# Kernel tuning notes

Hardware: AMD Instinct MI355X
Metric: run time of the kernel (lower is better)

The kernel has to match this reference:

```python
import jax, jax.numpy as jnp
import numpy as np

B, CIN, COUT, H, W, K = 4, 3, 16, 256, 256, 5
PAD = K // 2  # replicate padding keeps spatial size


def _dilation_sum(x, w):
    """Learnable dilation, channel_merge_mode='sum'.
    x: (B,Cin,H,W), w: (Cout,Cin,K,K).
    out[b,o,i,j] = sum_c max_{di,dj} ( x_pad[b,c,i+di,j+dj] + w[o,c,di,dj] )
    """
    xp = jnp.pad(x, ((0, 0), (0, 0), (PAD, PAD), (PAD, PAD)), mode='edge')
    acc = jnp.full((x.shape[0], w.shape[0], x.shape[1], H, W), -jnp.inf, dtype=x.dtype)
    for di in range(K):  # fixed small kernel loop (unrolled), not a data-dim loop
        for dj in range(K):
            win = xp[:, :, di:di + H, dj:dj + W]                     # (B,Cin,H,W)
            cand = win[:, None] + w[None, :, :, di, dj][:, :, :, None, None]  # (B,Cout,Cin,H,W)
            acc = jnp.maximum(acc, cand)
    return acc.sum(axis=2)  # merge over input channels -> (B,Cout,H,W)


def _erosion_identity(y, w):
    """Learnable erosion, channel_merge_mode='identity' (each channel independent).
    y: (B,Cout,H,W), w: (Cout,K,K).
    out[b,o,i,j] = min_{di,dj} ( y_pad[b,o,i+di,j+dj] - w[o,di,dj] )
    """
    yp = jnp.pad(y, ((0, 0), (0, 0), (PAD, PAD), (PAD, PAD)), mode='edge')
    acc = jnp.full(y.shape, jnp.inf, dtype=y.dtype)
    for di in range(K):
        for dj in range(K):
            acc = jnp.minimum(acc, yp[:, :, di:di + H, dj:dj + W] - w[None, :, di, dj, None, None])
    return acc


def setup_inputs() -> dict:
    key = jax.random.key(0)
    k1, k2, k3 = jax.random.split(key, 3)
    x = jax.random.normal(k1, (B, CIN, H, W), dtype=jnp.float32)
    w_d = jax.random.normal(k2, (COUT, CIN, K, K), dtype=jnp.float32) * 0.05
    w_e = jax.random.normal(k3, (COUT, K, K), dtype=jnp.float32) * 0.05
    return {"x": x, "w_d": w_d, "w_e": w_e}


def reference(x, w_d, w_e):
    # Closing = dilation (max-plus, sum merge) followed by erosion (min-plus, identity merge)
    dilated = _dilation_sum(x, w_d)
    return _erosion_identity(dilated, w_e)
```

## Files before the change

kernel.cpp:

```cpp
#include <hip/hip_runtime.h>


typedef _Float16 h2 __attribute__((ext_vector_type(2)));

namespace {
constexpr int HH = 256, WW = 256, CI = 3;
constexpr int XS2 = 36;
constexpr int CH2 = 68 * XS2;
constexpr int DS2 = 36;
}

struct __align__(16) H4  { h2 a, b, c, d; };
struct __align__(8)  H2p { h2 a, b; };

__device__ __forceinline__ h2 pmax(h2 a, h2 b) { return __builtin_elementwise_max(a, b); }
__device__ __forceinline__ h2 pmin(h2 a, h2 b) { return __builtin_elementwise_min(a, b); }

__device__ __forceinline__ h2 shr1(h2 lo, h2 hi) {
    unsigned a = __builtin_bit_cast(unsigned, lo);
    unsigned b = __builtin_bit_cast(unsigned, hi);
    return __builtin_bit_cast(h2, (a >> 16) | (b << 16));
}

__device__ __forceinline__ h2 splat2(float f) {
    auto p = __builtin_amdgcn_cvt_pkrtz(f, f);
    return __builtin_bit_cast(h2, p);
}

__device__ __forceinline__ void erode_one(int t, const h2* sd, const float* ew,
                                          float* outz, int i0, int j0) {
    const int r = t / 5, s = t - r * 5;
    const int eb = r * DS2 + 6 * s;
    h2 n0 = splat2(60000.f), n1 = n0, n2 = n0, n3 = n0, n4 = n0, n5 = n0;
#pragma unroll
    for (int r5 = 0; r5 < 5; ++r5) {
        const H2p q0 = *(const H2p*)&sd[eb + r5 * DS2];
        const H2p q1 = *(const H2p*)&sd[eb + r5 * DS2 + 2];
        const H2p q2 = *(const H2p*)&sd[eb + r5 * DS2 + 4];
        const H2p q3 = *(const H2p*)&sd[eb + r5 * DS2 + 6];
        const h2 e0 = q0.a, e1 = q0.b, e2 = q1.a, e3 = q1.b,
                 e4 = q2.a, e5 = q2.b, e6 = q3.a, e7 = q3.b;
        const h2 t0 = shr1(e0, e1), t1 = shr1(e1, e2), t2 = shr1(e2, e3),
                 t3 = shr1(e3, e4), t4 = shr1(e4, e5), t5 = shr1(e5, e6),
                 t6 = shr1(e6, e7);
        const h2 w0 = splat2(-ew[r5*5+0]), w1 = splat2(-ew[r5*5+1]),
                 w2 = splat2(-ew[r5*5+2]), w3 = splat2(-ew[r5*5+3]),
                 w4 = splat2(-ew[r5*5+4]);
        n0 = pmin(n0, pmin(pmin(e0 + w0, t0 + w1), pmin(e1 + w2, pmin(t1 + w3, e2 + w4))));
        n1 = pmin(n1, pmin(pmin(e1 + w0, t1 + w1), pmin(e2 + w2, pmin(t2 + w3, e3 + w4))));
        n2 = pmin(n2, pmin(pmin(e2 + w0, t2 + w1), pmin(e3 + w2, pmin(t3 + w3, e4 + w4))));
        n3 = pmin(n3, pmin(pmin(e3 + w0, t3 + w1), pmin(e4 + w2, pmin(t4 + w3, e5 + w4))));
        n4 = pmin(n4, pmin(pmin(e4 + w0, t4 + w1), pmin(e5 + w2, pmin(t5 + w3, e6 + w4))));
        n5 = pmin(n5, pmin(pmin(e5 + w0, t5 + w1), pmin(e6 + w2, pmin(t6 + w3, e7 + w4))));
    }
    float* op = outz + ((size_t)(i0 + r) << 8) + j0 + 12 * s;
    *(float4*)op       = make_float4((float)n0.x, (float)n0.y, (float)n1.x, (float)n1.y);
    *(float4*)(op + 4) = make_float4((float)n2.x, (float)n2.y, (float)n3.x, (float)n3.y);
    *(float4*)(op + 8) = make_float4((float)n4.x, (float)n4.y, (float)n5.x, (float)n5.y);
}

__global__ __launch_bounds__(256, 4)
void closing_v10(const float* __restrict__ x, const float* __restrict__ wd,
                 const float* __restrict__ we, float* __restrict__ out) {
    __shared__ __align__(16) h2 sx2[CI * CH2];
    __shared__ __align__(16) h2 sd2[64 * DS2];

    const int tid = threadIdx.x;
    const int bx = blockIdx.x, by = blockIdx.y, z = blockIdx.z;
    const int o = z & 15, b = z >> 4;
    const int i0 = min(by * 60, HH - 60);
    const int j0 = min(bx * 60, WW - 60);
    const float* xb = x + (size_t)b * (CI * HH * WW);

#pragma unroll
    for (int k = 0; k < 14; ++k) {
        const int idx = tid + (k << 8);
        if (idx < 3468) {
            const int c   = idx / 1156;
            const int rem = idx - c * 1156;
            const int r   = rem / 17;
            const int q   = rem - r * 17;
            const int gi  = min(max(i0 - 4 + r, 0), HH - 1);
            const int gj0 = j0 - 4 + (q << 2);
            const float* rowp = xb + c * (HH * WW) + (gi << 8);
            float4 v;
            if (gj0 < 0)        { const float t = rowp[0];      v = make_float4(t, t, t, t); }
            else if (gj0 > 252) { const float t = rowp[WW - 1]; v = make_float4(t, t, t, t); }
            else                  v = *(const float4*)(rowp + gj0);
            H2p hw;
            hw.a = h2{(_Float16)v.x, (_Float16)v.y};
            hw.b = h2{(_Float16)v.z, (_Float16)v.w};
            *(H2p*)&sx2[c * CH2 + r * XS2 + (q << 1)] = hw;
        }
    }
    __syncthreads();

    {
        const int r = tid >> 2, s = tid & 3;
        h2 acc0 = splat2(0.f), acc1 = acc0, acc2 = acc0, acc3 = acc0,
           acc4 = acc0, acc5 = acc0, acc6 = acc0, acc7 = acc0;
#pragma unroll
        for (int c = 0; c < CI; ++c) {
            const float* wr = wd + (o * CI + c) * 25;
            h2 m0 = splat2(-60000.f), m1 = m0, m2 = m0, m3 = m0,
               m4 = m0, m5 = m0, m6 = m0, m7 = m0;
            const int base = c * CH2 + r * XS2 + (s << 3);
#pragma unroll
            for (int r5 = 0; r5 < 5; ++r5) {
                const H4  A = *(const H4*)&sx2[base + r5 * XS2];
                const H4  B = *(const H4*)&sx2[base + r5 * XS2 + 4];
                const H2p C = *(const H2p*)&sx2[base + r5 * XS2 + 8];
                const h2 h0 = A.a, h1 = A.b, h2_ = A.c, h3 = A.d,
                         h4 = B.a, h5 = B.b, h6 = B.c, h7 = B.d,
                         h8 = C.a, h9 = C.b;
                const h2 t0 = shr1(h0, h1), t1 = shr1(h1, h2_), t2 = shr1(h2_, h3),
                         t3 = shr1(h3, h4), t4 = shr1(h4, h5), t5 = shr1(h5, h6),
                         t6 = shr1(h6, h7), t7 = shr1(h7, h8), t8 = shr1(h8, h9);
                const h2 w0 = splat2(wr[r5*5+0]), w1 = splat2(wr[r5*5+1]),
                         w2 = splat2(wr[r5*5+2]), w3 = splat2(wr[r5*5+3]),
                         w4 = splat2(wr[r5*5+4]);
                m0 = pmax(m0, pmax(pmax(h0 + w0, t0 + w1), pmax(h1 + w2, pmax(t1 + w3, h2_ + w4))));
                m1 = pmax(m1, pmax(pmax(h1 + w0, t1 + w1), pmax(h2_ + w2, pmax(t2 + w3, h3 + w4))));
                m2 = pmax(m2, pmax(pmax(h2_ + w0, t2 + w1), pmax(h3 + w2, pmax(t3 + w3, h4 + w4))));
                m3 = pmax(m3, pmax(pmax(h3 + w0, t3 + w1), pmax(h4 + w2, pmax(t4 + w3, h5 + w4))));
                m4 = pmax(m4, pmax(pmax(h4 + w0, t4 + w1), pmax(h5 + w2, pmax(t5 + w3, h6 + w4))));
                m5 = pmax(m5, pmax(pmax(h5 + w0, t5 + w1), pmax(h6 + w2, pmax(t6 + w3, h7 + w4))));
                m6 = pmax(m6, pmax(pmax(h6 + w0, t6 + w1), pmax(h7 + w2, pmax(t7 + w3, h8 + w4))));
                m7 = pmax(m7, pmax(pmax(h7 + w0, t7 + w1), pmax(h8 + w2, pmax(t8 + w3, h9 + w4))));
            }
            acc0 = acc0 + m0; acc1 = acc1 + m1; acc2 = acc2 + m2; acc3 = acc3 + m3;
            acc4 = acc4 + m4; acc5 = acc5 + m5; acc6 = acc6 + m6; acc7 = acc7 + m7;
        }
        if (j0 == 0       && s == 0) acc0 = (h2)acc1.x;
        if (j0 == WW - 60 && s == 3) acc7 = (h2)acc6.y;
        const bool top = (i0 == 0), bot = (i0 == HH - 60);
        if (!((top && r < 2) || (bot && r > 61))) {
            const H4 p0 = {acc0, acc1, acc2, acc3};
            const H4 p1 = {acc4, acc5, acc6, acc7};
            const int db = r * DS2 + (s << 3);
            *(H4*)&sd2[db]     = p0;
            *(H4*)&sd2[db + 4] = p1;
            if (top && r == 2) {
                *(H4*)&sd2[0 * DS2 + (s << 3)]     = p0;
                *(H4*)&sd2[0 * DS2 + (s << 3) + 4] = p1;
                *(H4*)&sd2[1 * DS2 + (s << 3)]     = p0;
                *(H4*)&sd2[1 * DS2 + (s << 3) + 4] = p1;
            }
            if (bot && r == 61) {
                *(H4*)&sd2[62 * DS2 + (s << 3)]     = p0;
                *(H4*)&sd2[62 * DS2 + (s << 3) + 4] = p1;
                *(H4*)&sd2[63 * DS2 + (s << 3)]     = p0;
                *(H4*)&sd2[63 * DS2 + (s << 3) + 4] = p1;
            }
        }
    }
    __syncthreads();

    {
        const float* ew = we + o * 25;
        float* outz = out + ((size_t)z << 16);
        erode_one(tid, sd2, ew, outz, i0, j0);
        if (tid < 44) erode_one(tid + 256, sd2, ew, outz, i0, j0);
    }
}

extern "C" void kernel_launch(void* const* d_in, const int* in_sizes, int n_in,
                              void* d_out, int out_size, void* d_ws, size_t ws_size,
                              hipStream_t stream) {
    const float* x  = (const float*)d_in[0];
    const float* wd = (const float*)d_in[1];
    const float* we = (const float*)d_in[2];
    float* out = (float*)d_out;

    dim3 grid(5, 5, 64);
    closing_v10<<<grid, dim3(256), 0, stream>>>(x, wd, we, out);
}
```

Measured before the change: 96.95 us.

## Shrink output tiles to 32x48 and rebalance per-thread work across stages

Output tiles shrink from 60x60 to 32 rows by 48 columns, so the grid grows from 5x5x64 to 6x8x64 blocks. The shared-memory buffers are resized to match. Each dilation thread now computes 4 packed pairs instead of 8, and each erosion thread computes 3 pairs instead of 6, so every thread does one erosion task rather than some doing a second. The aim is more blocks and a more even workload, with less per-thread register pressure and less tail imbalance. In exchange, more halo rows and columns are recomputed and reloaded relative to useful output, and the output stores become narrower float2 writes.

```diff
diff --git a/kernel.cpp b/kernel.cpp
--- a/kernel.cpp
+++ b/kernel.cpp
@@ -5,9 +5,9 @@
 
 namespace {
 constexpr int HH = 256, WW = 256, CI = 3;
-constexpr int XS2 = 36;
-constexpr int CH2 = 68 * XS2;
-constexpr int DS2 = 36;
+constexpr int XS2 = 28;
+constexpr int CH2 = 40 * XS2;
+constexpr int DS2 = 28;
 }
 
 struct __align__(16) H4  { h2 a, b, c, d; };
@@ -27,59 +27,27 @@
     return __builtin_bit_cast(h2, p);
 }
 
-__device__ __forceinline__ void erode_one(int t, const h2* sd, const float* ew,
-                                          float* outz, int i0, int j0) {
-    const int r = t / 5, s = t - r * 5;
-    const int eb = r * DS2 + 6 * s;
-    h2 n0 = splat2(60000.f), n1 = n0, n2 = n0, n3 = n0, n4 = n0, n5 = n0;
-#pragma unroll
-    for (int r5 = 0; r5 < 5; ++r5) {
-        const H2p q0 = *(const H2p*)&sd[eb + r5 * DS2];
-        const H2p q1 = *(const H2p*)&sd[eb + r5 * DS2 + 2];
-        const H2p q2 = *(const H2p*)&sd[eb + r5 * DS2 + 4];
-        const H2p q3 = *(const H2p*)&sd[eb + r5 * DS2 + 6];
-        const h2 e0 = q0.a, e1 = q0.b, e2 = q1.a, e3 = q1.b,
-                 e4 = q2.a, e5 = q2.b, e6 = q3.a, e7 = q3.b;
-        const h2 t0 = shr1(e0, e1), t1 = shr1(e1, e2), t2 = shr1(e2, e3),
-                 t3 = shr1(e3, e4), t4 = shr1(e4, e5), t5 = shr1(e5, e6),
-                 t6 = shr1(e6, e7);
-        const h2 w0 = splat2(-ew[r5*5+0]), w1 = splat2(-ew[r5*5+1]),
-                 w2 = splat2(-ew[r5*5+2]), w3 = splat2(-ew[r5*5+3]),
-                 w4 = splat2(-ew[r5*5+4]);
-        n0 = pmin(n0, pmin(pmin(e0 + w0, t0 + w1), pmin(e1 + w2, pmin(t1 + w3, e2 + w4))));
-        n1 = pmin(n1, pmin(pmin(e1 + w0, t1 + w1), pmin(e2 + w2, pmin(t2 + w3, e3 + w4))));
-        n2 = pmin(n2, pmin(pmin(e2 + w0, t2 + w1), pmin(e3 + w2, pmin(t3 + w3, e4 + w4))));
-        n3 = pmin(n3, pmin(pmin(e3 + w0, t3 + w1), pmin(e4 + w2, pmin(t4 + w3, e5 + w4))));
-        n4 = pmin(n4, pmin(pmin(e4 + w0, t4 + w1), pmin(e5 + w2, pmin(t5 + w3, e6 + w4))));
-        n5 = pmin(n5, pmin(pmin(e5 + w0, t5 + w1), pmin(e6 + w2, pmin(t6 + w3, e7 + w4))));
-    }
-    float* op = outz + ((size_t)(i0 + r) << 8) + j0 + 12 * s;
-    *(float4*)op       = make_float4((float)n0.x, (float)n0.y, (float)n1.x, (float)n1.y);
-    *(float4*)(op + 4) = make_float4((float)n2.x, (float)n2.y, (float)n3.x, (float)n3.y);
-    *(float4*)(op + 8) = make_float4((float)n4.x, (float)n4.y, (float)n5.x, (float)n5.y);
-}
-
 __global__ __launch_bounds__(256, 4)
-void closing_v10(const float* __restrict__ x, const float* __restrict__ wd,
+void closing_v13(const float* __restrict__ x, const float* __restrict__ wd,
                  const float* __restrict__ we, float* __restrict__ out) {
-    __shared__ __align__(16) h2 sx2[CI * CH2];
-    __shared__ __align__(16) h2 sd2[64 * DS2];
+    __shared__ __align__(16) h2 sx2[CI * CH2 + 8];
+    __shared__ __align__(16) h2 sd2[36 * DS2];
 
     const int tid = threadIdx.x;
     const int bx = blockIdx.x, by = blockIdx.y, z = blockIdx.z;
     const int o = z & 15, b = z >> 4;
-    const int i0 = min(by * 60, HH - 60);
-    const int j0 = min(bx * 60, WW - 60);
+    const int i0 = by * 32;
+    const int j0 = min(bx * 48, WW - 48);
     const float* xb = x + (size_t)b * (CI * HH * WW);
 
 #pragma unroll
-    for (int k = 0; k < 14; ++k) {
+    for (int k = 0; k < 7; ++k) {
         const int idx = tid + (k << 8);
-        if (idx < 3468) {
-            const int c   = idx / 1156;
-            const int rem = idx - c * 1156;
-            const int r   = rem / 17;
-            const int q   = rem - r * 17;
+        if (idx < 1680) {
+            const int c   = idx / 560;
+            const int rem = idx - c * 560;
+            const int r   = rem / 14;
+            const int q   = rem - r * 14;
             const int gi  = min(max(i0 - 4 + r, 0), HH - 1);
             const int gj0 = j0 - 4 + (q << 2);
             const float* rowp = xb + c * (HH * WW) + (gi << 8);
@@ -95,27 +63,21 @@
     }
     __syncthreads();
 
-    {
-        const int r = tid >> 2, s = tid & 3;
-        h2 acc0 = splat2(0.f), acc1 = acc0, acc2 = acc0, acc3 = acc0,
-           acc4 = acc0, acc5 = acc0, acc6 = acc0, acc7 = acc0;
+    if (tid < 252) {
+        const int r = tid / 7, s = tid - r * 7;
+        h2 acc0 = splat2(0.f), acc1 = acc0, acc2 = acc0, acc3 = acc0;
 #pragma unroll
         for (int c = 0; c < CI; ++c) {
             const float* wr = wd + (o * CI + c) * 25;
-            h2 m0 = splat2(-60000.f), m1 = m0, m2 = m0, m3 = m0,
-               m4 = m0, m5 = m0, m6 = m0, m7 = m0;
-            const int base = c * CH2 + r * XS2 + (s << 3);
+            h2 m0 = splat2(-60000.f), m1 = m0, m2 = m0, m3 = m0;
+            const int base = c * CH2 + r * XS2 + (s << 2);
 #pragma unroll
             for (int r5 = 0; r5 < 5; ++r5) {
                 const H4  A = *(const H4*)&sx2[base + r5 * XS2];
-                const H4  B = *(const H4*)&sx2[base + r5 * XS2 + 4];
-                const H2p C = *(const H2p*)&sx2[base + r5 * XS2 + 8];
-                const h2 h0 = A.a, h1 = A.b, h2_ = A.c, h3 = A.d,
-                         h4 = B.a, h5 = B.b, h6 = B.c, h7 = B.d,
-                         h8 = C.a, h9 = C.b;
+                const H2p B = *(const H2p*)&sx2[base + r5 * XS2 + 4];
+                const h2 h0 = A.a, h1 = A.b, h2_ = A.c, h3 = A.d, h4 = B.a, h5 = B.b;
                 const h2 t0 = shr1(h0, h1), t1 = shr1(h1, h2_), t2 = shr1(h2_, h3),
-                         t3 = shr1(h3, h4), t4 = shr1(h4, h5), t5 = shr1(h5, h6),
-                         t6 = shr1(h6, h7), t7 = shr1(h7, h8), t8 = shr1(h8, h9);
+                         t3 = shr1(h3, h4), t4 = shr1(h4, h5);
                 const h2 w0 = splat2(wr[r5*5+0]), w1 = splat2(wr[r5*5+1]),
                          w2 = splat2(wr[r5*5+2]), w3 = splat2(wr[r5*5+3]),
                          w4 = splat2(wr[r5*5+4]);
@@ -123,44 +85,61 @@
                 m1 = pmax(m1, pmax(pmax(h1 + w0, t1 + w1), pmax(h2_ + w2, pmax(t2 + w3, h3 + w4))));
                 m2 = pmax(m2, pmax(pmax(h2_ + w0, t2 + w1), pmax(h3 + w2, pmax(t3 + w3, h4 + w4))));
                 m3 = pmax(m3, pmax(pmax(h3 + w0, t3 + w1), pmax(h4 + w2, pmax(t4 + w3, h5 + w4))));
-                m4 = pmax(m4, pmax(pmax(h4 + w0, t4 + w1), pmax(h5 + w2, pmax(t5 + w3, h6 + w4))));
-                m5 = pmax(m5, pmax(pmax(h5 + w0, t5 + w1), pmax(h6 + w2, pmax(t6 + w3, h7 + w4))));
-                m6 = pmax(m6, pmax(pmax(h6 + w0, t6 + w1), pmax(h7 + w2, pmax(t7 + w3, h8 + w4))));
-                m7 = pmax(m7, pmax(pmax(h7 + w0, t7 + w1), pmax(h8 + w2, pmax(t8 + w3, h9 + w4))));
             }
             acc0 = acc0 + m0; acc1 = acc1 + m1; acc2 = acc2 + m2; acc3 = acc3 + m3;
-            acc4 = acc4 + m4; acc5 = acc5 + m5; acc6 = acc6 + m6; acc7 = acc7 + m7;
         }
         if (j0 == 0       && s == 0) acc0 = (h2)acc1.x;
-        if (j0 == WW - 60 && s == 3) acc7 = (h2)acc6.y;
-        const bool top = (i0 == 0), bot = (i0 == HH - 60);
-        if (!((top && r < 2) || (bot && r > 61))) {
-            const H4 p0 = {acc0, acc1, acc2, acc3};
-            const H4 p1 = {acc4, acc5, acc6, acc7};
-            const int db = r * DS2 + (s << 3);
-            *(H4*)&sd2[db]     = p0;
-            *(H4*)&sd2[db + 4] = p1;
+        if (j0 == WW - 48 && s == 6) acc1 = (h2)acc0.y;
+        const bool top = (by == 0), bot = (by == 7);
+        if (!((top && r < 2) || (bot && r > 33))) {
+            const int db = r * DS2 + (s << 2);
+            if (s < 6) { const H4 p = {acc0, acc1, acc2, acc3}; *(H4*)&sd2[db] = p; }
+            else       { const H2p p = {acc0, acc1};            *(H2p*)&sd2[db] = p; }
             if (top && r == 2) {
-                *(H4*)&sd2[0 * DS2 + (s << 3)]     = p0;
-                *(H4*)&sd2[0 * DS2 + (s << 3) + 4] = p1;
-                *(H4*)&sd2[1 * DS2 + (s << 3)]     = p0;
-                *(H4*)&sd2[1 * DS2 + (s << 3) + 4] = p1;
+                if (s < 6) { const H4 p = {acc0, acc1, acc2, acc3};
+                             *(H4*)&sd2[0 * DS2 + (s << 2)] = p;
+                             *(H4*)&sd2[1 * DS2 + (s << 2)] = p; }
+                else       { const H2p p = {acc0, acc1};
+                             *(H2p*)&sd2[0 * DS2 + (s << 2)] = p;
+                             *(H2p*)&sd2[1 * DS2 + (s << 2)] = p; }
             }
-            if (bot && r == 61) {
-                *(H4*)&sd2[62 * DS2 + (s << 3)]     = p0;
-                *(H4*)&sd2[62 * DS2 + (s << 3) + 4] = p1;
-                *(H4*)&sd2[63 * DS2 + (s << 3)]     = p0;
-                *(H4*)&sd2[63 * DS2 + (s << 3) + 4] = p1;
+            if (bot && r == 33) {
+                if (s < 6) { const H4 p = {acc0, acc1, acc2, acc3};
+                             *(H4*)&sd2[34 * DS2 + (s << 2)] = p;
+                             *(H4*)&sd2[35 * DS2 + (s << 2)] = p; }
+                else       { const H2p p = {acc0, acc1};
+                             *(H2p*)&sd2[34 * DS2 + (s << 2)] = p;
+                             *(H2p*)&sd2[35 * DS2 + (s << 2)] = p; }
             }
         }
     }
     __syncthreads();
 
     {
+        const int r = tid >> 3, s = tid & 7;
         const float* ew = we + o * 25;
-        float* outz = out + ((size_t)z << 16);
-        erode_one(tid, sd2, ew, outz, i0, j0);
-        if (tid < 44) erode_one(tid + 256, sd2, ew, outz, i0, j0);
+        const int eb = r * DS2 + 3 * s;
+        h2 n0 = splat2(60000.f), n1 = n0, n2 = n0;
+#pragma unroll
+        for (int r5 = 0; r5 < 5; ++r5) {
+            const h2 e0 = sd2[eb + r5 * DS2];
+            const h2 e1 = sd2[eb + r5 * DS2 + 1];
+            const h2 e2 = sd2[eb + r5 * DS2 + 2];
+            const h2 e3 = sd2[eb + r5 * DS2 + 3];
+            const h2 e4 = sd2[eb + r5 * DS2 + 4];
+            const h2 t0 = shr1(e0, e1), t1 = shr1(e1, e2), t2 = shr1(e2, e3),
+                     t3 = shr1(e3, e4);
+            const h2 w0 = splat2(-ew[r5*5+0]), w1 = splat2(-ew[r5*5+1]),
+                     w2 = splat2(-ew[r5*5+2]), w3 = splat2(-ew[r5*5+3]),
+                     w4 = splat2(-ew[r5*5+4]);
+            n0 = pmin(n0, pmin(pmin(e0 + w0, t0 + w1), pmin(e1 + w2, pmin(t1 + w3, e2 + w4))));
+            n1 = pmin(n1, pmin(pmin(e1 + w0, t1 + w1), pmin(e2 + w2, pmin(t2 + w3, e3 + w4))));
+            n2 = pmin(n2, pmin(pmin(e2 + w0, t2 + w1), pmin(e3 + w2, pmin(t3 + w3, e4 + w4))));
+        }
+        float* op = out + ((size_t)z << 16) + ((size_t)(i0 + r) << 8) + j0 + 6 * s;
+        *(float2*)op       = make_float2((float)n0.x, (float)n0.y);
+        *(float2*)(op + 2) = make_float2((float)n1.x, (float)n1.y);
+        *(float2*)(op + 4) = make_float2((float)n2.x, (float)n2.y);
     }
 }
 
@@ -172,6 +151,6 @@
     const float* we = (const float*)d_in[2];
     float* out = (float*)d_out;
 
-    dim3 grid(5, 5, 64);
-    closing_v10<<<grid, dim3(256), 0, stream>>>(x, wd, we, out);
+    dim3 grid(6, 8, 64);
+    closing_v13<<<grid, dim3(256), 0, stream>>>(x, wd, we, out);
 }
```

New measurement: 88.85 us. -8.4%, faster.
